# Optimization experiments

Measured on AMD Instinct MI355X. Metric: run time of the kernel, lower is better.

## Reference

```python
import jax, jax.numpy as jnp
import numpy as np

N, E, B = 50000, 800000, 64
F0, H, C = 8, 2, 64          # node feat dim, heads, per-head out dim
OBS, MH, NA = 128, 256, 16   # obs dim, mlp hidden, n_actions
NEG_SLOPE = 0.2


def setup_inputs() -> dict:
    key = jax.random.key(0)
    ks = jax.random.split(key, 30)
    p = lambda k, shape: (jax.random.normal(k, shape, dtype=jnp.float32) * 0.1)
    inp = {
        "obs": jax.random.normal(ks[0], (B, OBS), dtype=jnp.float32),
        "node_features": jax.random.normal(ks[1], (N, F0), dtype=jnp.float32),
        "edge_index": jax.random.randint(ks[2], (2, E), 0, N, dtype=jnp.int32),
        "batch": jnp.sort(jax.random.randint(ks[3], (N,), 0, B, dtype=jnp.int32)),
        # GAT layer 0: in=F0 -> heads=H, out=C, concat
        "W0": p(ks[4], (F0, H * C)), "a_src0": p(ks[5], (H, C)), "a_dst0": p(ks[6], (H, C)), "b0": p(ks[7], (H * C,)),
        # GAT layer 1: in=H*C -> heads=H, out=C, concat
        "W1": p(ks[8], (H * C, H * C)), "a_src1": p(ks[9], (H, C)), "a_dst1": p(ks[10], (H, C)), "b1": p(ks[11], (H * C,)),
        # GAT layer 2: in=H*C -> heads=1, out=C, no concat
        "W2": p(ks[12], (H * C, C)), "a_src2": p(ks[13], (1, C)), "a_dst2": p(ks[14], (1, C)), "b2": p(ks[15], (C,)),
        # MLP head: combined = C + OBS
        "Ws1": p(ks[16], (C + OBS, MH)), "bs1": p(ks[17], (MH,)),
        "ln_g": jnp.ones((MH,), jnp.float32), "ln_b": jnp.zeros((MH,), jnp.float32),
        "Ws2": p(ks[18], (MH, MH)), "bs2": p(ks[19], (MH,)),
        "Wa": p(ks[20], (MH, NA)), "ba": p(ks[21], (NA,)),
        "Wc": p(ks[22], (MH, 1)), "bc": p(ks[23], (1,)),
    }
    return inp


def gat_layer(x, src, dst, W, a_src, a_dst, bias, heads, out_dim, concat):
    n = x.shape[0]
    h = (x @ W).reshape(n, heads, out_dim)                     # [N,H,C]
    alpha_s = jnp.einsum("nhc,hc->nh", h, a_src)               # [N,H]
    alpha_d = jnp.einsum("nhc,hc->nh", h, a_dst)
    e = jax.nn.leaky_relu(alpha_s[src] + alpha_d[dst], NEG_SLOPE)  # [E,H]
    # scatter-softmax over incoming edges of each dst node (stable)
    emax = jax.ops.segment_max(e, dst, num_segments=n)
    ex = jnp.exp(e - emax[dst])
    denom = jax.ops.segment_sum(ex, dst, num_segments=n)
    alpha = ex / (denom[dst] + 1e-16)                          # [E,H]
    msg = h[src] * alpha[..., None]                            # [E,H,C]
    out = jax.ops.segment_sum(msg, dst, num_segments=n)        # [N,H,C]
    out = out.reshape(n, heads * out_dim) if concat else out.mean(axis=1)
    return out + bias


def reference(obs, node_features, edge_index, batch,
              W0, a_src0, a_dst0, b0, W1, a_src1, a_dst1, b1,
              W2, a_src2, a_dst2, b2,
              Ws1, bs1, ln_g, ln_b, Ws2, bs2, Wa, ba, Wc, bc):
    n = node_features.shape[0]
    # PyG GATConv default add_self_loops=True
    loop = jnp.arange(n, dtype=edge_index.dtype)
    src = jnp.concatenate([edge_index[0], loop])
    dst = jnp.concatenate([edge_index[1], loop])

    x = node_features
    x = jax.nn.elu(gat_layer(x, src, dst, W0, a_src0, a_dst0, b0, H, C, True))
    x = jax.nn.elu(gat_layer(x, src, dst, W1, a_src1, a_dst1, b1, H, C, True))
    x = gat_layer(x, src, dst, W2, a_src2, a_dst2, b2, 1, C, False)

    # global mean pool over graphs
    counts = jax.ops.segment_sum(jnp.ones((n,), x.dtype), batch, num_segments=B)
    pooled = jax.ops.segment_sum(x, batch, num_segments=B) / jnp.maximum(counts, 1.0)[:, None]

    combined = jnp.concatenate([pooled, obs], axis=-1)         # [B, C+OBS]
    h = combined @ Ws1 + bs1
    mu = h.mean(-1, keepdims=True)
    var = ((h - mu) ** 2).mean(-1, keepdims=True)
    h = (h - mu) / jnp.sqrt(var + 1e-5) * ln_g + ln_b
    h = jax.nn.relu(h)
    h = jax.nn.relu(h @ Ws2 + bs2)
    logits = h @ Wa + ba
    value = (h @ Wc + bc).squeeze(-1)
    return logits, value
```

## Files before the change

### kernel.cpp

```cpp
#include <hip/hip_runtime.h>
#include <math.h>


#define LRELU(x) ((x) > 0.f ? (x) : 0.2f * (x))

typedef short bf16x8 __attribute__((ext_vector_type(8)));
typedef unsigned short u16x8 __attribute__((ext_vector_type(8)));
typedef float f32x4 __attribute__((ext_vector_type(4)));
typedef float f32x2 __attribute__((ext_vector_type(2)));

__device__ __forceinline__ unsigned short f2bf(float f) {
    unsigned int u = __float_as_uint(f);
    u = (u + 0x7fffu + ((u >> 16) & 1u)) >> 16;
    return (unsigned short)u;
}
__device__ __forceinline__ float bf2f(unsigned short u) {
    return __uint_as_float((unsigned int)u << 16);
}
__device__ __forceinline__ unsigned char f2fp8(float f) {
    return (unsigned char)(__builtin_amdgcn_cvt_pk_fp8_f32(f, f, 0, false) & 0xff);
}
__device__ __forceinline__ f32x2 fp8pair(unsigned int u) {
    return __builtin_amdgcn_cvt_pk_f32_fp8(u, false);
}


__global__ __launch_bounds__(256) void hist_t0_kernel(
    const int* __restrict__ dst, int* __restrict__ histT,
    int e, int G1, int NB, int n, int hist_blocks, int t0_blocks, int wp_blocks,
    const float* __restrict__ x, const float* __restrict__ W,
    const float* __restrict__ a_src, const float* __restrict__ a_dst,
    unsigned char* __restrict__ h, float* __restrict__ as_o,
    float* __restrict__ ad_o,
    const float* __restrict__ W1, const float* __restrict__ W2,
    unsigned short* __restrict__ Wf1, unsigned short* __restrict__ Wf2,
    const int* __restrict__ batch, int* __restrict__ gstart, int nGraphs) {
    __shared__ unsigned int hist[256];
    __shared__ float xs[2][8][8];
    if ((int)blockIdx.x < hist_blocks) {
        hist[threadIdx.x] = 0;
        __syncthreads();
        int base = blockIdx.x * 2048 + threadIdx.x * 8;
        int d[8];
        if (base + 8 <= e) {
            int4 x0 = *(const int4*)(dst + base);
            int4 x1 = *(const int4*)(dst + base + 4);
            d[0] = x0.x; d[1] = x0.y; d[2] = x0.z; d[3] = x0.w;
            d[4] = x1.x; d[5] = x1.y; d[6] = x1.z; d[7] = x1.w;
        } else {
#pragma unroll
            for (int j = 0; j < 8; j++) {
                int ij = base + j;
                d[j] = (ij < e) ? dst[ij] : -1;
            }
        }
#pragma unroll
        for (int j = 0; j < 8; j++) {
            if (d[j] >= 0) atomicAdd(&hist[d[j] >> 8], 1u);
        }
        __syncthreads();
        int b = threadIdx.x;
        if (b < NB) histT[b * G1 + blockIdx.x] = (int)hist[b];
        return;
    }
    if ((int)blockIdx.x < hist_blocks + t0_blocks) {
        const int bid2 = blockIdx.x - hist_blocks;
        const int tid = threadIdx.x & 127;
        const int half = threadIdx.x >> 7;
        const int node0 = bid2 * 16 + half * 8;

        for (int idx = tid; idx < 64; idx += 128) {
            int ni = idx >> 3, k = idx & 7;
            int ng = node0 + ni;
            xs[half][ni][k] = (ng < n) ? x[(size_t)ng * 8 + k] : 0.f;
        }
        __syncthreads();

        float acc[8];
#pragma unroll
        for (int i = 0; i < 8; i++) acc[i] = 0.f;
#pragma unroll
        for (int k = 0; k < 8; k++) {
            float wk = W[k * 128 + tid];
#pragma unroll
            for (int i = 0; i < 8; i++) acc[i] += xs[half][i][k] * wk;
        }

        const int lane = tid & 63;
        const int head = tid >> 6;
        const int pos = 2 * lane + head;
        const float av = a_src[tid];
        const float dv = a_dst[tid];
#pragma unroll
        for (int i = 0; i < 8; i++) {
            int ng = node0 + i;
            if (ng >= n) break;
            h[(size_t)ng * 128 + pos] = f2fp8(acc[i]);
            float ps = acc[i] * av, pd = acc[i] * dv;
            for (int off = 32; off; off >>= 1) {
                ps += __shfl_xor(ps, off, 64);
                pd += __shfl_xor(pd, off, 64);
            }
            if (lane == 0) {
                as_o[ng * 2 + head] = ps;
                ad_o[ng * 2 + head] = pd;
            }
        }
        return;
    }
    if ((int)blockIdx.x < hist_blocks + t0_blocks + wp_blocks) {
        const int n1 = 8 * 4 * 64;
        const int n2 = 4 * 4 * 64;
        int gid = (blockIdx.x - hist_blocks - t0_blocks) * 256 + threadIdx.x;
        if (gid < n1) {
            int idx = gid;
            int lane = idx & 63, ts = idx >> 6;
            int s = ts & 3, t = ts >> 2;
            int quad = lane >> 4, cn = lane & 15;
#pragma unroll
            for (int j = 0; j < 8; j++)
                Wf1[idx * 8 + j] = f2bf(W1[(s * 32 + quad * 8 + j) * 128 + t * 16 + cn]);
        } else if (gid < n1 + n2) {
            int idx = gid - n1;
            int lane = idx & 63, ts = idx >> 6;
            int s = ts & 3, t = ts >> 2;
            int quad = lane >> 4, cn = lane & 15;
#pragma unroll
            for (int j = 0; j < 8; j++)
                Wf2[idx * 8 + j] = f2bf(W2[(s * 32 + quad * 8 + j) * 64 + t * 16 + cn]);
        }
        return;
    }
    int gid = (blockIdx.x - hist_blocks - t0_blocks - wp_blocks) * 256 + threadIdx.x;
    if (gid < n) {
        int bi = batch[gid];
        if (gid == 0) {
            for (int g = 0; g <= bi; g++) gstart[g] = 0;
        } else {
            int bp = batch[gid - 1];
            if (bi != bp)
                for (int g = bp + 1; g <= bi; g++) gstart[g] = gid;
        }
        if (gid == n - 1) {
            for (int g = bi + 1; g <= nGraphs; g++) gstart[g] = n;
        }
    }
}


__global__ __launch_bounds__(256) void scan2_block_kernel(
    const int* __restrict__ in, int* __restrict__ out,
    int* __restrict__ blockSums, int len) {
    __shared__ int lds[256];
    int t = threadIdx.x;
    int i0 = blockIdx.x * 512 + 2 * t;
    int v0 = (i0 < len) ? in[i0] : 0;
    int v1 = (i0 + 1 < len) ? in[i0 + 1] : 0;
    int s = v0 + v1;
    lds[t] = s;
    __syncthreads();
    for (int off = 1; off < 256; off <<= 1) {
        int u = (t >= off) ? lds[t - off] : 0;
        __syncthreads();
        lds[t] += u;
        __syncthreads();
    }
    int base = lds[t] - s;
    if (i0 < len) out[i0] = base;
    if (i0 + 1 < len) out[i0 + 1] = base + v0;
    if (t == 255) blockSums[blockIdx.x] = lds[255];
}

__global__ __launch_bounds__(256) void scan2_finalize_kernel(
    int* __restrict__ out, const int* __restrict__ blockSums, int len, int nb) {
    __shared__ int lds[256];
    int t = threadIdx.x;
    int v = (t < nb) ? blockSums[t] : 0;
    lds[t] = v;
    __syncthreads();
    for (int off = 1; off < 256; off <<= 1) {
        int u = (t >= off) ? lds[t - off] : 0;
        __syncthreads();
        lds[t] += u;
        __syncthreads();
    }
    const int bid = blockIdx.x;
    const int base = (bid > 0) ? lds[bid - 1] : 0;
    const int total = lds[nb - 1];
    int i0 = bid * 512 + 2 * t;
#pragma unroll
    for (int q = 0; q < 2; q++) {
        int i = i0 + q;
        if (i < len) out[i] += base;
        else if (i == len) out[len] = total;
    }
}


__global__ __launch_bounds__(256) void bucket_scatter_kernel(
    const int* __restrict__ src, const int* __restrict__ dst,
    const int* __restrict__ offs, int* __restrict__ esrc,
    unsigned char* __restrict__ dsub8, int e, int G1) {
    __shared__ unsigned int hist[256];
    hist[threadIdx.x] = 0;
    __syncthreads();
    int base = blockIdx.x * 2048 + threadIdx.x * 8;
    int d[8], s[8];
    if (base + 8 <= e) {
        int4 d0 = *(const int4*)(dst + base);
        int4 d1 = *(const int4*)(dst + base + 4);
        int4 s0 = *(const int4*)(src + base);
        int4 s1 = *(const int4*)(src + base + 4);
        d[0] = d0.x; d[1] = d0.y; d[2] = d0.z; d[3] = d0.w;
        d[4] = d1.x; d[5] = d1.y; d[6] = d1.z; d[7] = d1.w;
        s[0] = s0.x; s[1] = s0.y; s[2] = s0.z; s[3] = s0.w;
        s[4] = s1.x; s[5] = s1.y; s[6] = s1.z; s[7] = s1.w;
    } else {
#pragma unroll
        for (int j = 0; j < 8; j++) {
            int ij = base + j;
            bool v = ij < e;
            d[j] = v ? dst[ij] : -1;
            s[j] = v ? src[ij] : 0;
        }
    }
    unsigned lr[8];
#pragma unroll
    for (int j = 0; j < 8; j++) {
        lr[j] = (d[j] >= 0) ? atomicAdd(&hist[d[j] >> 8], 1u) : 0u;
    }
#pragma unroll
    for (int j = 0; j < 8; j++) {
        if (d[j] >= 0) {
            int pos = offs[(d[j] >> 8) * G1 + blockIdx.x] + (int)lr[j];
            esrc[pos] = s[j];
            dsub8[pos] = (unsigned char)(d[j] & 255);
        }
    }
}


__global__ __launch_bounds__(256) void bucket_csr_kernel(
    const int* __restrict__ offs, const unsigned char* __restrict__ dsub8,
    const int* __restrict__ esrc, int* __restrict__ row_ptr,
    int* __restrict__ col, int G1, int n) {
    __shared__ unsigned int cnt[256];
    __shared__ int rp[256];
    int t = threadIdx.x;
    int b = blockIdx.x;
    cnt[t] = 0;
    __syncthreads();
    int bs = offs[b * G1];
    int be = offs[(b + 1) * G1];
    for (int i = bs + t; i < be; i += 256) {
        atomicAdd(&cnt[dsub8[i]], 1u);
    }
    __syncthreads();
    int v = (int)cnt[t];
    rp[t] = v;
    __syncthreads();
    for (int off = 1; off < 256; off <<= 1) {
        int u = (t >= off) ? rp[t - off] : 0;
        __syncthreads();
        rp[t] += u;
        __syncthreads();
    }
    int excl = rp[t] - v;
    int node = b * 256 + t;
    if (node <= n) row_ptr[node] = bs + excl;
    __syncthreads();
    cnt[t] = (unsigned)excl;
    __syncthreads();
    for (int i = bs + t; i < be; i += 256) {
        int sub = dsub8[i];
        unsigned r = atomicAdd(&cnt[sub], 1u);
        col[bs + (int)r] = esrc[i];
    }
}

template <int OUT, int HEADS>
__device__ __forceinline__ int hpos8(int c) {
    return (HEADS == 2) ? (2 * (c & 63) + (c >> 6)) : c;
}


template <int OUT, int HEADS>
__global__ __launch_bounds__(256) void transform_mfma_kernel(
    const unsigned short* __restrict__ xb, const unsigned short* __restrict__ Wf,
    const float* __restrict__ a_src, const float* __restrict__ a_dst,
    unsigned char* __restrict__ h, float* __restrict__ as_o, float* __restrict__ ad_o,
    int n) {
    constexpr int T = OUT / 16, S = 4;
    const int w = threadIdx.x >> 6, lane = threadIdx.x & 63;
    const int node0 = (blockIdx.x * 4 + w) * 16;
    if (node0 >= n) return;
    const int quad = lane >> 4, col = lane & 15;

    const int arow = node0 + col;
    const bool aok = arow < n;
    bf16x8 a[S];
    const unsigned short* xrow = xb + (size_t)arow * 128 + quad * 8;
#pragma unroll
    for (int s = 0; s < S; s++) {
        bf16x8 z = {0, 0, 0, 0, 0, 0, 0, 0};
        a[s] = aok ? *(const bf16x8*)(xrow + s * 32) : z;
    }

    f32x4 acc[T];
#pragma unroll
    for (int t = 0; t < T; t++) acc[t] = (f32x4){0.f, 0.f, 0.f, 0.f};

#pragma unroll
    for (int s = 0; s < S; s++) {
#pragma unroll
        for (int t = 0; t < T; t++) {
            bf16x8 b = *(const bf16x8*)(Wf + ((size_t)(t * S + s) * 64 + lane) * 8);
            acc[t] = __builtin_amdgcn_mfma_f32_16x16x32_bf16(a[s], b, acc[t], 0, 0, 0);
        }
    }

#pragma unroll
    for (int t = 0; t < T; t++) {
        int pos = hpos8<OUT, HEADS>(t * 16 + col);
#pragma unroll
        for (int r = 0; r < 4; r++) {
            int m = node0 + quad * 4 + r;
            if (m < n) h[(size_t)m * OUT + pos] = f2fp8(acc[t][r]);
        }
    }

#pragma unroll
    for (int r = 0; r < 4; r++) {
        float s0 = 0.f, s1 = 0.f, d0 = 0.f, d1 = 0.f;
#pragma unroll
        for (int t = 0; t < T; t++) {
            float av = a_src[t * 16 + col];
            float dv = a_dst[t * 16 + col];
            float v = acc[t][r];
            if (HEADS == 2 && t >= T / 2) { s1 += v * av; d1 += v * dv; }
            else                          { s0 += v * av; d0 += v * dv; }
        }
        for (int off = 8; off; off >>= 1) {
            s0 += __shfl_xor(s0, off, 64);
            d0 += __shfl_xor(d0, off, 64);
            if (HEADS == 2) {
                s1 += __shfl_xor(s1, off, 64);
                d1 += __shfl_xor(d1, off, 64);
            }
        }
        int m = node0 + quad * 4 + r;
        if (m < n) {
            if (HEADS == 2) {
                if (col == 0)      { as_o[m * 2] = s0;     ad_o[m * 2] = d0; }
                else if (col == 1) { as_o[m * 2 + 1] = s1; ad_o[m * 2 + 1] = d1; }
            } else {
                if (col == 0) { as_o[m] = s0; ad_o[m] = d0; }
            }
        }
    }
}


template <int ACT>
__global__ __launch_bounds__(256) void agg2_kernel(
    const int* __restrict__ row_ptr, const int* __restrict__ col,
    const unsigned char* __restrict__ h, const float2* __restrict__ as2,
    const float2* __restrict__ ad2, const float* __restrict__ bias,
    unsigned short* __restrict__ out, int n) {
    __shared__ float w0l[4][2][32], w1l[4][2][32];
    __shared__ unsigned sofl[4][2][32];
    const int w = threadIdx.x >> 6;
    const int lane = threadIdx.x & 63;
    const int half = lane >> 5, l = lane & 31;
    const int node = blockIdx.x * 8 + w * 2 + half;
    const bool active = node < n;

    int beg = 0, deg = 0;
    float2 adv = make_float2(0.f, 0.f);
    float den0 = 0.f, den1 = 0.f;
    float a0 = 0.f, a1 = 0.f, a2 = 0.f, a3 = 0.f;
    if (active) {
        beg = row_ptr[node];
        deg = row_ptr[node + 1] - beg;
        adv = ad2[node];
        float2 avs = as2[node];
        float w0s = __expf(LRELU(avs.x + adv.x));
        float w1s = __expf(LRELU(avs.y + adv.y));
        unsigned us = *(const unsigned*)(h + ((size_t)node << 7) + 4 * l);
        f32x2 p0 = fp8pair(us & 0xffffu);
        f32x2 p1 = fp8pair(us >> 16);
        a0 = w0s * p0.x; a1 = w1s * p0.y;
        a2 = w0s * p1.x; a3 = w1s * p1.y;
        den0 = w0s; den1 = w1s;
    }
    int dmax = deg;
    for (int off = 32; off; off >>= 1) dmax = max(dmax, __shfl_xor(dmax, off, 64));

    for (int base = 0; base < dmax; base += 32) {
        int cnt = deg - base;
        cnt = cnt < 0 ? 0 : (cnt > 32 ? 32 : cnt);
        float w0 = 0.f, w1 = 0.f;
        unsigned so = 0;
        if (l < cnt) {
            int s = col[beg + base + l];
            float2 av = as2[s];
            w0 = __expf(LRELU(av.x + adv.x));
            w1 = __expf(LRELU(av.y + adv.y));
            so = (unsigned)s << 7;
        }
        float t0 = w0, t1 = w1;
        for (int off = 16; off; off >>= 1) {
            t0 += __shfl_xor(t0, off, 64);
            t1 += __shfl_xor(t1, off, 64);
        }
        den0 += t0; den1 += t1;
        w0l[w][half][l] = w0;
        w1l[w][half][l] = w1;
        sofl[w][half][l] = so;

        int jmax = dmax - base;
        jmax = jmax > 32 ? 32 : jmax;
        for (int j = 0; j < jmax; j += 8) {
            unsigned u[8];
#pragma unroll
            for (int k = 0; k < 8; k++) {
                unsigned so_k = sofl[w][half][j + k];
                u[k] = *(const unsigned*)(h + so_k + 4 * l);
            }
            float W0[8], W1[8];
#pragma unroll
            for (int k = 0; k < 8; k++) {
                W0[k] = w0l[w][half][j + k];
                W1[k] = w1l[w][half][j + k];
            }
#pragma unroll
            for (int k = 0; k < 8; k++) {
                f32x2 p0 = fp8pair(u[k] & 0xffffu);
                f32x2 p1 = fp8pair(u[k] >> 16);
                a0 += W0[k] * p0.x; a1 += W1[k] * p0.y;
                a2 += W0[k] * p1.x; a3 += W1[k] * p1.y;
            }
        }
    }

    if (active) {
        float2 bA = *(const float2*)(bias + 2 * l);
        float2 bB = *(const float2*)(bias + 64 + 2 * l);
        float r0 = 1.f / (den0 + 1e-16f), r1 = 1.f / (den1 + 1e-16f);
        float o0 = a0 * r0 + bA.x;
        float o1 = a1 * r1 + bB.x;
        float o2 = a2 * r0 + bA.y;
        float o3 = a3 * r1 + bB.y;
        if (ACT) {
            o0 = o0 > 0.f ? o0 : expm1f(o0);
            o1 = o1 > 0.f ? o1 : expm1f(o1);
            o2 = o2 > 0.f ? o2 : expm1f(o2);
            o3 = o3 > 0.f ? o3 : expm1f(o3);
        }
        unsigned h0 = (unsigned)f2bf(o0) | ((unsigned)f2bf(o2) << 16);
        unsigned h1 = (unsigned)f2bf(o1) | ((unsigned)f2bf(o3) << 16);
        *(unsigned*)(out + (size_t)node * 128 + 2 * l) = h0;
        *(unsigned*)(out + (size_t)node * 128 + 64 + 2 * l) = h1;
    }
}


__global__ __launch_bounds__(256) void agg1_kernel(
    const int* __restrict__ row_ptr, const int* __restrict__ col,
    const unsigned char* __restrict__ h, const float* __restrict__ as1,
    const float* __restrict__ ad1, const float* __restrict__ bias,
    unsigned short* __restrict__ out, int n) {
    __shared__ float wl[4][2][32];
    __shared__ unsigned sofl[4][2][32];
    const int w = threadIdx.x >> 6;
    const int lane = threadIdx.x & 63;
    const int half = lane >> 5, l = lane & 31;
    const int node = blockIdx.x * 8 + w * 2 + half;
    const bool active = node < n;

    int beg = 0, deg = 0;
    float adv = 0.f, den = 0.f, a0 = 0.f, a2 = 0.f;
    if (active) {
        beg = row_ptr[node];
        deg = row_ptr[node + 1] - beg;
        adv = ad1[node];
        float ws = __expf(LRELU(as1[node] + adv));
        unsigned us = *(const unsigned short*)(h + ((size_t)node << 6) + 2 * l);
        f32x2 p = fp8pair(us);
        a0 = ws * p.x;
        a2 = ws * p.y;
        den = ws;
    }
    int dmax = deg;
    for (int off = 32; off; off >>= 1) dmax = max(dmax, __shfl_xor(dmax, off, 64));

    for (int base = 0; base < dmax; base += 32) {
        int cnt = deg - base;
        cnt = cnt < 0 ? 0 : (cnt > 32 ? 32 : cnt);
        float w0 = 0.f;
        unsigned so = 0;
        if (l < cnt) {
            int s = col[beg + base + l];
            w0 = __expf(LRELU(as1[s] + adv));
            so = (unsigned)s << 6;
        }
        float t = w0;
        for (int off = 16; off; off >>= 1) t += __shfl_xor(t, off, 64);
        den += t;
        wl[w][half][l] = w0;
        sofl[w][half][l] = so;

        int jmax = dmax - base;
        jmax = jmax > 32 ? 32 : jmax;
        for (int j = 0; j < jmax; j += 8) {
            unsigned u[8];
#pragma unroll
            for (int k = 0; k < 8; k++) {
                unsigned so_k = sofl[w][half][j + k];
                u[k] = *(const unsigned short*)(h + so_k + 2 * l);
            }
            float W0[8];
#pragma unroll
            for (int k = 0; k < 8; k++) W0[k] = wl[w][half][j + k];
#pragma unroll
            for (int k = 0; k < 8; k++) {
                f32x2 p = fp8pair(u[k]);
                a0 += W0[k] * p.x;
                a2 += W0[k] * p.y;
            }
        }
    }

    if (active) {
        float2 bA = *(const float2*)(bias + 2 * l);
        float r = 1.f / (den + 1e-16f);
        float o0 = a0 * r + bA.x;
        float o2 = a2 * r + bA.y;
        unsigned hv = (unsigned)f2bf(o0) | ((unsigned)f2bf(o2) << 16);
        *(unsigned*)(out + (size_t)node * 64 + 2 * l) = hv;
    }
}


__global__ __launch_bounds__(512) void mlp_kernel(
    const unsigned short* __restrict__ xbuf, const int* __restrict__ gstart,
    const float* __restrict__ obs,
    const float* __restrict__ Ws1, const float* __restrict__ bs1,
    const float* __restrict__ ln_g, const float* __restrict__ ln_b,
    const float* __restrict__ Ws2, const float* __restrict__ bs2,
    const float* __restrict__ Wa, const float* __restrict__ ba,
    const float* __restrict__ Wc, const float* __restrict__ bc,
    float* __restrict__ out_logits, float* __restrict__ out_value) {
    int b = blockIdx.x;
    int t = threadIdx.x;
    __shared__ float comb[192];
    __shared__ float red[512];
    __shared__ float red2[8][64];
    __shared__ float hs[256];

    const int gs = gstart[b];
    const int ge = gstart[b + 1];

    {
        const int w = t >> 6, lane = t & 63;
        const int rg = w * 8 + (lane >> 3);
        const int sub = lane & 7;
        float acc[8];
#pragma unroll
        for (int j = 0; j < 8; j++) acc[j] = 0.f;
        for (int i = gs + rg; i < ge; i += 64) {
            u16x8 v = *(const u16x8*)(xbuf + (size_t)i * 64 + sub * 8);
#pragma unroll
            for (int j = 0; j < 8; j++) acc[j] += bf2f(v[j]);
        }
#pragma unroll
        for (int off = 8; off <= 32; off <<= 1) {
#pragma unroll
            for (int j = 0; j < 8; j++) acc[j] += __shfl_xor(acc[j], off, 64);
        }
        if (lane < 8) {
#pragma unroll
            for (int j = 0; j < 8; j++) red2[w][lane * 8 + j] = acc[j];
        }
    }
    __syncthreads();
    {
        float cdiv = fmaxf((float)(ge - gs), 1.f);
        if (t < 64) {
            float s = 0.f;
#pragma unroll
            for (int w = 0; w < 8; w++) s += red2[w][t];
            comb[t] = s / cdiv;
        } else if (t < 192) {
            comb[t] = obs[b * 128 + (t - 64)];
        }
    }
    __syncthreads();

    const int t256 = t & 255;
    const int khalf = t >> 8;

    {
        float accA = 0.f, accB = 0.f;
        int k0 = khalf * 96;
#pragma unroll 4
        for (int k = k0; k < k0 + 96; k += 2) {
            accA += comb[k] * Ws1[k * 256 + t256];
            accB += comb[k + 1] * Ws1[(k + 1) * 256 + t256];
        }
        red[t] = accA + accB;
    }
    __syncthreads();
    float acc = 0.f;
    if (t < 256) acc = bs1[t] + red[t] + red[t + 256];
    __syncthreads();

    red[t] = (t < 256) ? acc : 0.f;
    __syncthreads();
    for (int off = 128; off; off >>= 1) {
        if (t < off) red[t] += red[t + off];
        __syncthreads();
    }
    float mu = red[0] / 256.f;
    __syncthreads();
    float d = acc - mu;
    red[t] = (t < 256) ? d * d : 0.f;
    __syncthreads();
    for (int off = 128; off; off >>= 1) {
        if (t < off) red[t] += red[t + off];
        __syncthreads();
    }
    float var = red[0] / 256.f;
    if (t < 256) {
        float hn = d * rsqrtf(var + 1e-5f) * ln_g[t] + ln_b[t];
        hs[t] = hn > 0.f ? hn : 0.f;
    }
    __syncthreads();

    {
        float a2A = 0.f, a2B = 0.f;
        int k0 = khalf * 128;
#pragma unroll 4
        for (int k = k0; k < k0 + 128; k += 2) {
            a2A += hs[k] * Ws2[k * 256 + t256];
            a2B += hs[k + 1] * Ws2[(k + 1) * 256 + t256];
        }
        red[t] = a2A + a2B;
    }
    __syncthreads();
    float acc2 = 0.f;
    if (t < 256) {
        acc2 = bs2[t] + red[t] + red[t + 256];
        acc2 = acc2 > 0.f ? acc2 : 0.f;
    }
    __syncthreads();
    if (t < 256) hs[t] = acc2;
    __syncthreads();

    {
        int o = t & 15, ck = t >> 4;
        float p = 0.f;
#pragma unroll
        for (int k = 0; k < 8; k++)
            p += hs[ck * 8 + k] * Wa[(ck * 8 + k) * 16 + o];
        red[t] = p;
    }
    __syncthreads();
    for (int off = 16; off >= 1; off >>= 1) {
        if ((t >> 4) < off) red[t] += red[t + off * 16];
        __syncthreads();
    }
    if (t < 16) out_logits[b * 16 + t] = red[t] + ba[t];
    __syncthreads();

    red[t] = (t < 256) ? hs[t] * Wc[t] : 0.f;
    __syncthreads();
    for (int off = 256; off; off >>= 1) {
        if (t < off) red[t] += red[t + off];
        __syncthreads();
    }
    if (t == 0) out_value[b] = red[0] + bc[0];
}


extern "C" void kernel_launch(void* const* d_in, const int* in_sizes, int n_in,
                              void* d_out, int out_size, void* d_ws, size_t ws_size,
                              hipStream_t stream) {
    const float* obs    = (const float*)d_in[0];
    const float* nf     = (const float*)d_in[1];
    const int*   ei     = (const int*)d_in[2];
    const int*   batch  = (const int*)d_in[3];
    const float* W0     = (const float*)d_in[4];
    const float* a_src0 = (const float*)d_in[5];
    const float* a_dst0 = (const float*)d_in[6];
    const float* b0     = (const float*)d_in[7];
    const float* W1     = (const float*)d_in[8];
    const float* a_src1 = (const float*)d_in[9];
    const float* a_dst1 = (const float*)d_in[10];
    const float* b1     = (const float*)d_in[11];
    const float* W2     = (const float*)d_in[12];
    const float* a_src2 = (const float*)d_in[13];
    const float* a_dst2 = (const float*)d_in[14];
    const float* b2     = (const float*)d_in[15];
    const float* Ws1    = (const float*)d_in[16];
    const float* bs1    = (const float*)d_in[17];
    const float* ln_g   = (const float*)d_in[18];
    const float* ln_b   = (const float*)d_in[19];
    const float* Ws2    = (const float*)d_in[20];
    const float* bs2    = (const float*)d_in[21];
    const float* Wa     = (const float*)d_in[22];
    const float* ba     = (const float*)d_in[23];
    const float* Wc     = (const float*)d_in[24];
    const float* bc     = (const float*)d_in[25];

    const int N = in_sizes[3];
    const int E = in_sizes[2] / 2;
    const int B = in_sizes[0] / 128;
    const int* src = ei;
    const int* dstp = ei + E;

    char* p = (char*)d_ws;
    auto alloc = [&](size_t bytes) -> void* {
        void* r = (void*)p;
        p += (bytes + 255) & ~(size_t)255;
        return r;
    };
    const int G1 = (E + 2047) / 2048;
    const int NB = (N + 255) >> 8;
    const int L  = NB * G1;
    int*   row_ptr   = (int*)alloc((size_t)(N + 1) * 4);
    int*   col       = (int*)alloc((size_t)E * 4);
    int*   esrc      = (int*)alloc((size_t)E * 4);
    unsigned char* dsub8 = (unsigned char*)alloc((size_t)E);
    int*   histT     = (int*)alloc((size_t)L * 4);
    int*   offs      = (int*)alloc((size_t)(L + 1) * 4);
    unsigned char* hbuf = (unsigned char*)alloc((size_t)N * 128);
    unsigned short* xb = (unsigned short*)alloc((size_t)N * 128 * 2);
    unsigned short* xbuf = (unsigned short*)alloc((size_t)N * 64 * 2);
    float* as_       = (float*)alloc((size_t)N * 2 * 4);
    float* ad_       = (float*)alloc((size_t)N * 2 * 4);
    unsigned short* Wf1 = (unsigned short*)alloc((size_t)8 * 4 * 64 * 8 * 2);
    unsigned short* Wf2 = (unsigned short*)alloc((size_t)4 * 4 * 64 * 8 * 2);
    int* gstart      = (int*)alloc((size_t)(B + 1) * 4);
    int* blockSums = (int*)xb;

    float* out_logits = (float*)d_out;
    float* out_value  = out_logits + (size_t)B * 16;

    int t0_blocks = (N + 15) / 16;
    int wp_blocks = (8 * 4 * 64 + 4 * 4 * 64 + 255) / 256;
    int gb_blocks = (N + 255) / 256;
    hist_t0_kernel<<<G1 + t0_blocks + wp_blocks + gb_blocks, 256, 0, stream>>>(
        dstp, histT, E, G1, NB, N, G1, t0_blocks, wp_blocks,
        nf, W0, a_src0, a_dst0, hbuf, as_, ad_,
        W1, W2, Wf1, Wf2, batch, gstart, B);

    int nbA = (L + 511) / 512;
    scan2_block_kernel<<<nbA, 256, 0, stream>>>(histT, offs, blockSums, L);
    scan2_finalize_kernel<<<(L + 1 + 511) / 512, 256, 0, stream>>>(offs, blockSums, L, nbA);

    bucket_scatter_kernel<<<G1, 256, 0, stream>>>(src, dstp, offs, esrc, dsub8, E, G1);
    bucket_csr_kernel<<<NB, 256, 0, stream>>>(offs, dsub8, esrc, row_ptr, col, G1, N);

    agg2_kernel<1><<<(N + 7) / 8, 256, 0, stream>>>(
        row_ptr, col, hbuf, (const float2*)as_, (const float2*)ad_, b0, xb, N);

    transform_mfma_kernel<128, 2><<<(N + 63) / 64, 256, 0, stream>>>(
        xb, Wf1, a_src1, a_dst1, hbuf, as_, ad_, N);
    agg2_kernel<1><<<(N + 7) / 8, 256, 0, stream>>>(
        row_ptr, col, hbuf, (const float2*)as_, (const float2*)ad_, b1, xb, N);

    transform_mfma_kernel<64, 1><<<(N + 63) / 64, 256, 0, stream>>>(
        xb, Wf2, a_src2, a_dst2, hbuf, as_, ad_, N);
    agg1_kernel<<<(N + 7) / 8, 256, 0, stream>>>(
        row_ptr, col, hbuf, as_, ad_, b2, xbuf, N);

    mlp_kernel<<<B, 512, 0, stream>>>(xbuf, gstart, obs, Ws1, bs1, ln_g, ln_b,
                                      Ws2, bs2, Wa, ba, Wc, bc,
                                      out_logits, out_value);
}
```

Measured before the change: 265.5 us.

## Fold histogram scan into bucket scatter and shrink buckets to 128 nodes

Removes the two separate scan kernels by having each bucket_scatter block compute its own per-bucket prefix offsets directly from the histogram table, read row by row. Histogram blocks now cover 8192 edges instead of 2048, and buckets now cover 128 nodes instead of 256, giving 391 buckets handled with 512-entry shared arrays. This saves two kernel launches and their global round trips. In exchange, every scatter block redundantly reads and reduces the whole histogram table, and fewer, larger scatter blocks reduce parallelism.

```diff
diff --git a/kernel.cpp b/kernel.cpp
--- a/kernel.cpp
+++ b/kernel.cpp
@@ -35,38 +35,38 @@
     const float* __restrict__ W1, const float* __restrict__ W2,
     unsigned short* __restrict__ Wf1, unsigned short* __restrict__ Wf2,
     const int* __restrict__ batch, int* __restrict__ gstart, int nGraphs) {
-    __shared__ unsigned int hist[256];
+    __shared__ unsigned int hist[512];
     __shared__ float xs[2][8][8];
+    const int t = threadIdx.x;
     if ((int)blockIdx.x < hist_blocks) {
-        hist[threadIdx.x] = 0;
-        __syncthreads();
-        int base = blockIdx.x * 2048 + threadIdx.x * 8;
-        int d[8];
-        if (base + 8 <= e) {
-            int4 x0 = *(const int4*)(dst + base);
-            int4 x1 = *(const int4*)(dst + base + 4);
-            d[0] = x0.x; d[1] = x0.y; d[2] = x0.z; d[3] = x0.w;
-            d[4] = x1.x; d[5] = x1.y; d[6] = x1.z; d[7] = x1.w;
-        } else {
-#pragma unroll
-            for (int j = 0; j < 8; j++) {
-                int ij = base + j;
-                d[j] = (ij < e) ? dst[ij] : -1;
-            }
-        }
-#pragma unroll
-        for (int j = 0; j < 8; j++) {
-            if (d[j] >= 0) atomicAdd(&hist[d[j] >> 8], 1u);
-        }
-        __syncthreads();
-        int b = threadIdx.x;
-        if (b < NB) histT[b * G1 + blockIdx.x] = (int)hist[b];
+        hist[t] = 0;
+        hist[t + 256] = 0;
+        __syncthreads();
+        const int g = blockIdx.x;
+#pragma unroll
+        for (int jj = 0; jj < 8; jj++) {
+            int idx = g * 8192 + jj * 1024 + t * 4;
+            int d[4];
+            if (idx + 4 <= e) {
+                int4 dd = *(const int4*)(dst + idx);
+                d[0] = dd.x; d[1] = dd.y; d[2] = dd.z; d[3] = dd.w;
+            } else {
+#pragma unroll
+                for (int q = 0; q < 4; q++) d[q] = (idx + q < e) ? dst[idx + q] : -1;
+            }
+#pragma unroll
+            for (int q = 0; q < 4; q++)
+                if (d[q] >= 0) atomicAdd(&hist[d[q] >> 7], 1u);
+        }
+        __syncthreads();
+        if (t < NB) histT[g * NB + t] = (int)hist[t];
+        if (t + 256 < NB) histT[g * NB + t + 256] = (int)hist[t + 256];
         return;
     }
     if ((int)blockIdx.x < hist_blocks + t0_blocks) {
         const int bid2 = blockIdx.x - hist_blocks;
-        const int tid = threadIdx.x & 127;
-        const int half = threadIdx.x >> 7;
+        const int tid = t & 127;
+        const int half = t >> 7;
         const int node0 = bid2 * 16 + half * 8;
 
         for (int idx = tid; idx < 64; idx += 128) {
@@ -111,27 +111,27 @@
     if ((int)blockIdx.x < hist_blocks + t0_blocks + wp_blocks) {
         const int n1 = 8 * 4 * 64;
         const int n2 = 4 * 4 * 64;
-        int gid = (blockIdx.x - hist_blocks - t0_blocks) * 256 + threadIdx.x;
+        int gid = (blockIdx.x - hist_blocks - t0_blocks) * 256 + t;
         if (gid < n1) {
             int idx = gid;
             int lane = idx & 63, ts = idx >> 6;
-            int s = ts & 3, t = ts >> 2;
+            int s = ts & 3, tt = ts >> 2;
             int quad = lane >> 4, cn = lane & 15;
 #pragma unroll
             for (int j = 0; j < 8; j++)
-                Wf1[idx * 8 + j] = f2bf(W1[(s * 32 + quad * 8 + j) * 128 + t * 16 + cn]);
+                Wf1[idx * 8 + j] = f2bf(W1[(s * 32 + quad * 8 + j) * 128 + tt * 16 + cn]);
         } else if (gid < n1 + n2) {
             int idx = gid - n1;
             int lane = idx & 63, ts = idx >> 6;
-            int s = ts & 3, t = ts >> 2;
+            int s = ts & 3, tt = ts >> 2;
             int quad = lane >> 4, cn = lane & 15;
 #pragma unroll
             for (int j = 0; j < 8; j++)
-                Wf2[idx * 8 + j] = f2bf(W2[(s * 32 + quad * 8 + j) * 64 + t * 16 + cn]);
+                Wf2[idx * 8 + j] = f2bf(W2[(s * 32 + quad * 8 + j) * 64 + tt * 16 + cn]);
         }
         return;
     }
-    int gid = (blockIdx.x - hist_blocks - t0_blocks - wp_blocks) * 256 + threadIdx.x;
+    int gid = (blockIdx.x - hist_blocks - t0_blocks - wp_blocks) * 256 + t;
     if (gid < n) {
         int bi = batch[gid];
         if (gid == 0) {
@@ -148,128 +148,116 @@
 }
 
 
-__global__ __launch_bounds__(256) void scan2_block_kernel(
-    const int* __restrict__ in, int* __restrict__ out,
-    int* __restrict__ blockSums, int len) {
-    __shared__ int lds[256];
-    int t = threadIdx.x;
-    int i0 = blockIdx.x * 512 + 2 * t;
-    int v0 = (i0 < len) ? in[i0] : 0;
-    int v1 = (i0 + 1 < len) ? in[i0 + 1] : 0;
-    int s = v0 + v1;
-    lds[t] = s;
-    __syncthreads();
-    for (int off = 1; off < 256; off <<= 1) {
-        int u = (t >= off) ? lds[t - off] : 0;
-        __syncthreads();
-        lds[t] += u;
-        __syncthreads();
-    }
-    int base = lds[t] - s;
-    if (i0 < len) out[i0] = base;
-    if (i0 + 1 < len) out[i0 + 1] = base + v0;
-    if (t == 255) blockSums[blockIdx.x] = lds[255];
-}
-
-__global__ __launch_bounds__(256) void scan2_finalize_kernel(
-    int* __restrict__ out, const int* __restrict__ blockSums, int len, int nb) {
-    __shared__ int lds[256];
-    int t = threadIdx.x;
-    int v = (t < nb) ? blockSums[t] : 0;
-    lds[t] = v;
-    __syncthreads();
-    for (int off = 1; off < 256; off <<= 1) {
-        int u = (t >= off) ? lds[t - off] : 0;
-        __syncthreads();
-        lds[t] += u;
-        __syncthreads();
-    }
-    const int bid = blockIdx.x;
-    const int base = (bid > 0) ? lds[bid - 1] : 0;
-    const int total = lds[nb - 1];
-    int i0 = bid * 512 + 2 * t;
-#pragma unroll
-    for (int q = 0; q < 2; q++) {
-        int i = i0 + q;
-        if (i < len) out[i] += base;
-        else if (i == len) out[len] = total;
-    }
-}
-
-
 __global__ __launch_bounds__(256) void bucket_scatter_kernel(
     const int* __restrict__ src, const int* __restrict__ dst,
-    const int* __restrict__ offs, int* __restrict__ esrc,
-    unsigned char* __restrict__ dsub8, int e, int G1) {
-    __shared__ unsigned int hist[256];
-    hist[threadIdx.x] = 0;
-    __syncthreads();
-    int base = blockIdx.x * 2048 + threadIdx.x * 8;
-    int d[8], s[8];
-    if (base + 8 <= e) {
-        int4 d0 = *(const int4*)(dst + base);
-        int4 d1 = *(const int4*)(dst + base + 4);
-        int4 s0 = *(const int4*)(src + base);
-        int4 s1 = *(const int4*)(src + base + 4);
-        d[0] = d0.x; d[1] = d0.y; d[2] = d0.z; d[3] = d0.w;
-        d[4] = d1.x; d[5] = d1.y; d[6] = d1.z; d[7] = d1.w;
-        s[0] = s0.x; s[1] = s0.y; s[2] = s0.z; s[3] = s0.w;
-        s[4] = s1.x; s[5] = s1.y; s[6] = s1.z; s[7] = s1.w;
-    } else {
-#pragma unroll
-        for (int j = 0; j < 8; j++) {
-            int ij = base + j;
-            bool v = ij < e;
-            d[j] = v ? dst[ij] : -1;
-            s[j] = v ? src[ij] : 0;
-        }
-    }
-    unsigned lr[8];
-#pragma unroll
-    for (int j = 0; j < 8; j++) {
-        lr[j] = (d[j] >= 0) ? atomicAdd(&hist[d[j] >> 8], 1u) : 0u;
-    }
-#pragma unroll
-    for (int j = 0; j < 8; j++) {
-        if (d[j] >= 0) {
-            int pos = offs[(d[j] >> 8) * G1 + blockIdx.x] + (int)lr[j];
-            esrc[pos] = s[j];
-            dsub8[pos] = (unsigned char)(d[j] & 255);
+    const int* __restrict__ histT, int* __restrict__ esrc,
+    unsigned char* __restrict__ dsub8, int* __restrict__ prefA,
+    int e, int G1, int NB) {
+    __shared__ int totL[512], scn[256], prefL[512], baseL[512];
+    __shared__ unsigned cnt[512];
+    const int t = threadIdx.x;
+    const int g = blockIdx.x;
+
+    int p0 = 0, tt0 = 0, p1 = 0, tt1 = 0;
+    const bool hasHi = (t + 256) < NB;
+    for (int g2 = 0; g2 < G1; g2++) {
+        int v0 = (t < NB) ? histT[g2 * NB + t] : 0;
+        int v1 = hasHi ? histT[g2 * NB + t + 256] : 0;
+        if (g2 < g) { p0 += v0; p1 += v1; }
+        tt0 += v0; tt1 += v1;
+    }
+    totL[t] = (t < NB) ? tt0 : 0;
+    totL[t + 256] = hasHi ? tt1 : 0;
+    __syncthreads();
+    int v0 = totL[2 * t], v1 = totL[2 * t + 1];
+    int s = v0 + v1;
+    scn[t] = s;
+    __syncthreads();
+    for (int off = 1; off < 256; off <<= 1) {
+        int u = (t >= off) ? scn[t - off] : 0;
+        __syncthreads();
+        scn[t] += u;
+        __syncthreads();
+    }
+    int base2 = scn[t] - s;
+    prefL[2 * t] = base2;
+    prefL[2 * t + 1] = base2 + v0;
+    __syncthreads();
+    baseL[t] = prefL[t] + p0;
+    baseL[t + 256] = prefL[t + 256] + p1;
+    cnt[t] = 0;
+    cnt[t + 256] = 0;
+    if (g == 0) {
+        if (t < NB) prefA[t] = prefL[t];
+        if (hasHi) prefA[t + 256] = prefL[t + 256];
+        if (t == 0) prefA[NB] = scn[255];
+    }
+    __syncthreads();
+
+#pragma unroll
+    for (int jj = 0; jj < 8; jj++) {
+        int idx = g * 8192 + jj * 1024 + t * 4;
+        int d[4], sv[4];
+        if (idx + 4 <= e) {
+            int4 dd = *(const int4*)(dst + idx);
+            int4 ss = *(const int4*)(src + idx);
+            d[0] = dd.x; d[1] = dd.y; d[2] = dd.z; d[3] = dd.w;
+            sv[0] = ss.x; sv[1] = ss.y; sv[2] = ss.z; sv[3] = ss.w;
+        } else {
+#pragma unroll
+            for (int q = 0; q < 4; q++) {
+                bool v = idx + q < e;
+                d[q] = v ? dst[idx + q] : -1;
+                sv[q] = v ? src[idx + q] : 0;
+            }
+        }
+        unsigned r[4];
+#pragma unroll
+        for (int q = 0; q < 4; q++)
+            r[q] = (d[q] >= 0) ? atomicAdd(&cnt[d[q] >> 7], 1u) : 0u;
+#pragma unroll
+        for (int q = 0; q < 4; q++) {
+            if (d[q] >= 0) {
+                int pos = baseL[d[q] >> 7] + (int)r[q];
+                esrc[pos] = sv[q];
+                dsub8[pos] = (unsigned char)(d[q] & 127);
+            }
         }
     }
 }
 
 
 __global__ __launch_bounds__(256) void bucket_csr_kernel(
-    const int* __restrict__ offs, const unsigned char* __restrict__ dsub8,
+    const int* __restrict__ prefA, const unsigned char* __restrict__ dsub8,
     const int* __restrict__ esrc, int* __restrict__ row_ptr,
-    int* __restrict__ col, int G1, int n) {
-    __shared__ unsigned int cnt[256];
-    __shared__ int rp[256];
-    int t = threadIdx.x;
-    int b = blockIdx.x;
-    cnt[t] = 0;
-    __syncthreads();
-    int bs = offs[b * G1];
-    int be = offs[(b + 1) * G1];
+    int* __restrict__ col, int n) {
+    __shared__ unsigned int cnt[128];
+    __shared__ int rp[128];
+    const int t = threadIdx.x;
+    const int b = blockIdx.x;
+    const int bs = prefA[b];
+    const int be = prefA[b + 1];
+    if (t < 128) cnt[t] = 0;
+    __syncthreads();
     for (int i = bs + t; i < be; i += 256) {
         atomicAdd(&cnt[dsub8[i]], 1u);
     }
     __syncthreads();
-    int v = (int)cnt[t];
-    rp[t] = v;
-    __syncthreads();
-    for (int off = 1; off < 256; off <<= 1) {
-        int u = (t >= off) ? rp[t - off] : 0;
-        __syncthreads();
-        rp[t] += u;
-        __syncthreads();
-    }
-    int excl = rp[t] - v;
-    int node = b * 256 + t;
-    if (node <= n) row_ptr[node] = bs + excl;
-    __syncthreads();
-    cnt[t] = (unsigned)excl;
+    int v = 0;
+    if (t < 128) { v = (int)cnt[t]; rp[t] = v; }
+    __syncthreads();
+    for (int off = 1; off < 128; off <<= 1) {
+        int u = (t >= off && t < 128) ? rp[t - off] : 0;
+        __syncthreads();
+        if (t < 128) rp[t] += u;
+        __syncthreads();
+    }
+    if (t < 128) {
+        int excl = rp[t] - v;
+        int node = b * 128 + t;
+        if (node <= n) row_ptr[node] = bs + excl;
+        cnt[t] = (unsigned)excl;
+    }
     __syncthreads();
     for (int i = bs + t; i < be; i += 256) {
         int sub = dsub8[i];
@@ -725,15 +713,14 @@
         p += (bytes + 255) & ~(size_t)255;
         return r;
     };
-    const int G1 = (E + 2047) / 2048;
-    const int NB = (N + 255) >> 8;
-    const int L  = NB * G1;
+    const int G1 = (E + 8191) / 8192;
+    const int NB = (N + 127) >> 7;
     int*   row_ptr   = (int*)alloc((size_t)(N + 1) * 4);
     int*   col       = (int*)alloc((size_t)E * 4);
     int*   esrc      = (int*)alloc((size_t)E * 4);
     unsigned char* dsub8 = (unsigned char*)alloc((size_t)E);
-    int*   histT     = (int*)alloc((size_t)L * 4);
-    int*   offs      = (int*)alloc((size_t)(L + 1) * 4);
+    int*   histT     = (int*)alloc((size_t)G1 * NB * 4);
+    int*   prefA     = (int*)alloc((size_t)(NB + 1) * 4);
     unsigned char* hbuf = (unsigned char*)alloc((size_t)N * 128);
     unsigned short* xb = (unsigned short*)alloc((size_t)N * 128 * 2);
     unsigned short* xbuf = (unsigned short*)alloc((size_t)N * 64 * 2);
@@ -742,7 +729,6 @@
     unsigned short* Wf1 = (unsigned short*)alloc((size_t)8 * 4 * 64 * 8 * 2);
     unsigned short* Wf2 = (unsigned short*)alloc((size_t)4 * 4 * 64 * 8 * 2);
     int* gstart      = (int*)alloc((size_t)(B + 1) * 4);
-    int* blockSums = (int*)xb;
 
     float* out_logits = (float*)d_out;
     float* out_value  = out_logits + (size_t)B * 16;
@@ -755,12 +741,10 @@
         nf, W0, a_src0, a_dst0, hbuf, as_, ad_,
         W1, W2, Wf1, Wf2, batch, gstart, B);
 
-    int nbA = (L + 511) / 512;
-    scan2_block_kernel<<<nbA, 256, 0, stream>>>(histT, offs, blockSums, L);
-    scan2_finalize_kernel<<<(L + 1 + 511) / 512, 256, 0, stream>>>(offs, blockSums, L, nbA);
-
-    bucket_scatter_kernel<<<G1, 256, 0, stream>>>(src, dstp, offs, esrc, dsub8, E, G1);
-    bucket_csr_kernel<<<NB, 256, 0, stream>>>(offs, dsub8, esrc, row_ptr, col, G1, N);
+    bucket_scatter_kernel<<<G1, 256, 0, stream>>>(
+        src, dstp, histT, esrc, dsub8, prefA, E, G1, NB);
+    bucket_csr_kernel<<<NB, 256, 0, stream>>>(
+        prefA, dsub8, esrc, row_ptr, col, N);
 
     agg2_kernel<1><<<(N + 7) / 8, 256, 0, stream>>>(
         row_ptr, col, hbuf, (const float2*)as_, (const float2*)ad_, b0, xb, N);
```

After: 288.6 us. 8.7% more time.
